# Performance work log

Hardware: AMD Instinct MI355X
Metric: run time of the kernel (lower is better)

## Reference

```python
import jax, jax.numpy as jnp
import numpy as np

DIMS = [1024, 2048, 1024, 1024]


def setup_inputs() -> dict:
    key = jax.random.key(0)
    ks = jax.random.split(key, 13)
    d_in, h1, h2, d_out = DIMS
    s = lambda k, shape, fan_in: jax.random.normal(k, shape, dtype=jnp.float32) / np.sqrt(fan_in)
    return {
        "x": jax.random.normal(ks[0], (4, 2048, d_in), dtype=jnp.float32),
        "w1": s(ks[1], (h1, d_in), d_in), "b1": jnp.zeros((h1,), jnp.float32),
        "w2": s(ks[2], (h2, h1), h1), "b2": jnp.zeros((h2,), jnp.float32),
        "wq": s(ks[3], (h2, h2), h2), "bq": jnp.zeros((h2,), jnp.float32),
        "wk": s(ks[4], (h2, h2), h2), "bk": jnp.zeros((h2,), jnp.float32),
        "wv": s(ks[5], (h2, h2), h2), "bv": jnp.zeros((h2,), jnp.float32),
        "wo": s(ks[6], (d_out, h2), h2), "bo": jnp.zeros((d_out,), jnp.float32),
    }


def reference(x, w1, b1, w2, b2, wq, bq, wk, bk, wv, bv, wo, bo):
    # MLP: Linear + ReLU twice (torch Linear: x @ W^T + b)
    h = jax.nn.relu(jnp.einsum('bsd,hd->bsh', x, w1) + b1)
    h = jax.nn.relu(jnp.einsum('bsh,eh->bse', h, w2) + b2)
    # Self-attention (single head over full hidden_dim)
    q = jnp.einsum('bse,fe->bsf', h, wq) + bq
    k = jnp.einsum('bse,fe->bsf', h, wk) + bk
    v = jnp.einsum('bse,fe->bsf', h, wv) + bv
    hidden_dim = wq.shape[0]
    scores = jnp.einsum('bsf,btf->bst', q, k) / jnp.sqrt(jnp.float32(hidden_dim))
    attn = jax.nn.softmax(scores, axis=-1)
    ctx = jnp.einsum('bst,btf->bsf', attn, v) + v  # residual with V
    return jnp.einsum('bsf,of->bso', ctx, wo) + bo
```

## Files before the change

### kernel.cpp

```cpp
#include <hip/hip_runtime.h>
#include <hip/hip_bf16.h>

typedef __bf16 bf16;
typedef bf16 bf16x8 __attribute__((ext_vector_type(8)));
typedef float f32x4 __attribute__((ext_vector_type(4)));

#define EPI_BIAS_RELU  0
#define EPI_BIAS_BF16  1
#define EPI_PLAIN_BF16 2
#define EPI_RESID      3
#define EPI_BIAS_F32   4

__device__ __forceinline__ void lds_load16(const bf16* g, bf16* l) {
  __builtin_amdgcn_global_load_lds((__attribute__((address_space(1))) void*)g,
                                   (__attribute__((address_space(3))) void*)l,
                                   16, 0, 0);
}

template<int N> __device__ __forceinline__ void vmw() {
  if constexpr (N == 0) asm volatile("s_waitcnt vmcnt(0)" ::: "memory");
  else if constexpr (N == 2) asm volatile("s_waitcnt vmcnt(2)" ::: "memory");
  else if constexpr (N == 4) asm volatile("s_waitcnt vmcnt(4)" ::: "memory");
  else if constexpr (N == 6) asm volatile("s_waitcnt vmcnt(6)" ::: "memory");
}
__device__ __forceinline__ void barrier() { asm volatile("s_barrier" ::: "memory"); }

__device__ __forceinline__ void xcd_map(int& bx, int& by, int& z) {
  const int gx = gridDim.x, gy = gridDim.y;
  const int Y8 = (gy * gridDim.z) >> 3;
  const int L = (blockIdx.z * gy + blockIdx.y) * gx + blockIdx.x;
  const int xcd = L & 7, j = L >> 3;
  bx = j % gx;
  const int yy = xcd * Y8 + j / gx;
  by = yy % gy;
  z  = yy / gy;
}

template<int EPI>
__global__ __launch_bounds__(512, 2)
void gemm4p(const bf16* __restrict__ A, const bf16* __restrict__ B,
            void* __restrict__ Cv, const float* __restrict__ bias,
            int K, int lda, int ldb, int ldc,
            long long sAz, long long sBz, long long sCz)
{
  constexpr int BM = 256, BK = 64;
  constexpr int M_REP = 8, N_REP = 4, MH = 4, NH = 2;
  constexpr int LA = 2, LB = 2, N3 = LA + LB + LA;

  __shared__ __align__(16) bf16 lA[2][BM * BK];
  __shared__ __align__(16) bf16 lB[2][256 * BK];

  int bx, by, z;
  xcd_map(bx, by, z);

  const bf16* Ab = A + (size_t)z * sAz;
  const bf16* Bb = B + (size_t)z * sBz;
  const int row0 = by * BM, col0 = bx * 256;
  const int tid = threadIdx.x, w = tid >> 6, l = tid & 63;
  const int wr = w >> 2, wc = w & 3;

  const int srow = l >> 3, scb = (l & 7) ^ srow;
  const bf16* gA = Ab + (size_t)(row0 + w * 8 + srow) * lda + scb * 8;
  const bf16* gB = Bb + (size_t)(col0 + w * 8 + srow) * ldb + scb * 8;

  auto issueA = [&](int buf, int k0, int h) {
#pragma unroll
    for (int i = 0; i < LA; i++)
      lds_load16(gA + (size_t)(h * 128 + i * 64) * lda + k0,
                 &lA[buf][(h * 128 + i * 64 + w * 8) * BK]);
  };
  auto issueB = [&](int buf, int k0, int h) {
#pragma unroll
    for (int i = 0; i < LB; i++)
      lds_load16(gB + (size_t)(h * 128 + i * 64) * ldb + k0,
                 &lB[buf][(h * 128 + i * 64 + w * 8) * BK]);
  };

  const int fr = l & 15, fq = l >> 4, sw = fr & 7;
  bf16x8 aA0[MH][2], aA1[MH][2], bB0[NH][2], bB1[NH][2];
  f32x4 acc[M_REP][N_REP] = {};

  auto readA = [&](bf16x8 (&dst)[MH][2], int buf, int h) {
#pragma unroll
    for (int mm = 0; mm < MH; mm++) {
      const bf16* base = &lA[buf][(h * 128 + wr * 64 + mm * 16 + fr) * BK];
#pragma unroll
      for (int kk = 0; kk < 2; kk++)
        dst[mm][kk] = *(const bf16x8*)(base + ((kk * 4 + fq) ^ sw) * 8);
    }
  };
  auto readB = [&](bf16x8 (&dst)[NH][2], int buf, int h) {
#pragma unroll
    for (int nn = 0; nn < NH; nn++) {
      const bf16* base = &lB[buf][(h * 128 + wc * 32 + nn * 16 + fr) * BK];
#pragma unroll
      for (int kk = 0; kk < 2; kk++)
        dst[nn][kk] = *(const bf16x8*)(base + ((kk * 4 + fq) ^ sw) * 8);
    }
  };
  auto quad = [&](const bf16x8 (&a)[MH][2], const bf16x8 (&b)[NH][2],
                  int mBase, int nBase) {
    __builtin_amdgcn_s_setprio(1);
#pragma unroll
    for (int mh = 0; mh < MH; mh++)
#pragma unroll
      for (int nh = 0; nh < NH; nh++)
#pragma unroll
        for (int kk = 0; kk < 2; kk++)
          acc[mBase + mh][nBase + nh] = __builtin_amdgcn_mfma_f32_16x16x32_bf16(
              a[mh][kk], b[nh][kk], acc[mBase + mh][nBase + nh], 0, 0, 0);
    __builtin_amdgcn_s_setprio(0);
  };

  const int NT = K / BK;
  issueA(0, 0, 0); issueB(0, 0, 0); issueA(0, 0, 1); issueB(0, 0, 1);
  issueA(1, BK, 0); issueB(1, BK, 0); issueA(1, BK, 1);
  vmw<N3>();
  barrier();

  for (int t = 0; t < NT; t++) {
    const int cur = t & 1, nxt = cur ^ 1;
    const bool s1 = (t + 1 < NT), s2 = (t + 2 < NT);
    const int k1 = (t + 1) * BK, k2 = (t + 2) * BK;
    readA(aA0, cur, 0);
    readB(bB0, cur, 0);
    if (s1) issueB(nxt, k1, 1);
    barrier();
    quad(aA0, bB0, 0, 0);
    barrier();
    readA(aA1, cur, 1);
    if (s2) issueA(cur, k2, 0);
    barrier();
    quad(aA1, bB0, MH, 0);
    barrier();
    readB(bB1, cur, 1);
    if (s2) issueB(cur, k2, 0);
    barrier();
    quad(aA1, bB1, MH, NH);
    barrier();
    if (s2) { issueA(cur, k2, 1); vmw<N3>(); }
    else vmw<0>();
    barrier();
    quad(aA0, bB1, 0, NH);
    barrier();
  }

#pragma unroll
  for (int m = 0; m < M_REP; m++) {
#pragma unroll
    for (int n = 0; n < N_REP; n++) {
      const int col = col0 + (n / NH) * 128 + wc * 32 + (n % NH) * 16 + fr;
#pragma unroll
      for (int j = 0; j < 4; j++) {
        const int rrow = row0 + (m / MH) * 128 + wr * 64 + (m % MH) * 16 + fq * 4 + j;
        const float val = acc[m][n][j];
        if constexpr (EPI == EPI_PLAIN_BF16) {
          bf16* Cp = (bf16*)Cv + (size_t)z * sCz;
          Cp[(size_t)rrow * ldc + col] = (bf16)val;
        } else if constexpr (EPI == EPI_BIAS_BF16) {
          bf16* Cp = (bf16*)Cv;
          Cp[(size_t)rrow * ldc + col] = (bf16)(val + bias[col]);
        } else if constexpr (EPI == EPI_BIAS_RELU) {
          bf16* Cp = (bf16*)Cv;
          Cp[(size_t)rrow * ldc + col] = (bf16)fmaxf(val + bias[col], 0.f);
        }
      }
    }
  }
}

template<int EPI>
__global__ __launch_bounds__(512, 2)
void gemm2p(const bf16* __restrict__ A, const bf16* __restrict__ B,
            void* __restrict__ Cv, const float* __restrict__ bias,
            const bf16* __restrict__ resid,
            int K, int lda, int ldb, int ldc, int ldr,
            long long sAz, long long sBz, long long sCz, long long sRz)
{
  constexpr int BM = 128, BK = 64;
  constexpr int M_REP = 4, NH = 2;

  __shared__ __align__(16) bf16 lA[2][BM * BK];
  __shared__ __align__(16) bf16 lB[2][256 * BK];

  int bx, by, z;
  xcd_map(bx, by, z);

  const bf16* Ab = A + (size_t)z * sAz;
  const bf16* Bb = B + (size_t)z * sBz;
  const int row0 = by * BM, col0 = bx * 256;
  const int tid = threadIdx.x, w = tid >> 6, l = tid & 63;
  const int wr = w >> 2, wc = w & 3;

  const int srow = l >> 3, scb = (l & 7) ^ srow;
  const bf16* gA = Ab + (size_t)(row0 + w * 8 + srow) * lda + scb * 8;
  const bf16* gB = Bb + (size_t)(col0 + w * 8 + srow) * ldb + scb * 8;

  auto issueAfull = [&](int buf, int k0) {
#pragma unroll
    for (int i = 0; i < 2; i++)
      lds_load16(gA + (size_t)(i * 64) * lda + k0,
                 &lA[buf][(i * 64 + w * 8) * BK]);
  };
  auto issueBfull = [&](int buf, int k0) {
#pragma unroll
    for (int i = 0; i < 4; i++)
      lds_load16(gB + (size_t)(i * 64) * ldb + k0,
                 &lB[buf][(i * 64 + w * 8) * BK]);
  };

  const int fr = l & 15, fq = l >> 4, sw = fr & 7;
  bf16x8 aA[M_REP][2], bB0[NH][2], bB1[NH][2];
  f32x4 acc[M_REP][4] = {};

  auto readAfull = [&](int buf) {
#pragma unroll
    for (int m = 0; m < M_REP; m++) {
      const bf16* base = &lA[buf][(wr * 64 + m * 16 + fr) * BK];
#pragma unroll
      for (int kk = 0; kk < 2; kk++)
        aA[m][kk] = *(const bf16x8*)(base + ((kk * 4 + fq) ^ sw) * 8);
    }
  };
  auto readB = [&](bf16x8 (&dst)[NH][2], int buf, int h) {
#pragma unroll
    for (int nn = 0; nn < NH; nn++) {
      const bf16* base = &lB[buf][(h * 128 + wc * 32 + nn * 16 + fr) * BK];
#pragma unroll
      for (int kk = 0; kk < 2; kk++)
        dst[nn][kk] = *(const bf16x8*)(base + ((kk * 4 + fq) ^ sw) * 8);
    }
  };
  auto quad2 = [&](const bf16x8 (&b)[NH][2], int nBase) {
    __builtin_amdgcn_s_setprio(1);
#pragma unroll
    for (int m = 0; m < M_REP; m++)
#pragma unroll
      for (int nh = 0; nh < NH; nh++)
#pragma unroll
        for (int kk = 0; kk < 2; kk++)
          acc[m][nBase + nh] = __builtin_amdgcn_mfma_f32_16x16x32_bf16(
              aA[m][kk], b[nh][kk], acc[m][nBase + nh], 0, 0, 0);
    __builtin_amdgcn_s_setprio(0);
  };

  const int NT = K / BK;
  issueAfull(0, 0); issueBfull(0, 0); issueAfull(1, BK);
  vmw<2>();
  barrier();

  for (int t = 0; t < NT; t++) {
    const int cur = t & 1, nxt = cur ^ 1;
    const bool s1 = (t + 1 < NT), s2 = (t + 2 < NT);
    readAfull(cur);
    readB(bB0, cur, 0);
    if (s1) issueBfull(nxt, (t + 1) * BK);
    barrier();
    quad2(bB0, 0);
    barrier();
    readB(bB1, cur, 1);
    if (s2) { issueAfull(cur, (t + 2) * BK); vmw<2>(); }
    else vmw<0>();
    barrier();
    quad2(bB1, NH);
    barrier();
  }

#pragma unroll
  for (int m = 0; m < M_REP; m++) {
#pragma unroll
    for (int n = 0; n < 4; n++) {
      const int col = col0 + (n / NH) * 128 + wc * 32 + (n % NH) * 16 + fr;
#pragma unroll
      for (int j = 0; j < 4; j++) {
        const int rrow = row0 + wr * 64 + m * 16 + fq * 4 + j;
        const float val = acc[m][n][j];
        if constexpr (EPI == EPI_PLAIN_BF16) {
          bf16* Cp = (bf16*)Cv + (size_t)z * sCz;
          Cp[(size_t)rrow * ldc + col] = (bf16)val;
        } else if constexpr (EPI == EPI_BIAS_F32) {
          float* Cp = (float*)Cv;
          Cp[(size_t)rrow * ldc + col] = val + bias[col];
        } else if constexpr (EPI == EPI_BIAS_BF16) {
          bf16* Cp = (bf16*)Cv;
          Cp[(size_t)rrow * ldc + col] = (bf16)(val + bias[col]);
        } else if constexpr (EPI == EPI_BIAS_RELU) {
          bf16* Cp = (bf16*)Cv;
          Cp[(size_t)rrow * ldc + col] = (bf16)fmaxf(val + bias[col], 0.f);
        } else {
          bf16* Cp = (bf16*)Cv + (size_t)z * sCz;
          const bf16* Rp = resid + (size_t)z * sRz;
          Cp[(size_t)rrow * ldc + col] = (bf16)(val + (float)Rp[(size_t)rrow * ldr + col]);
        }
      }
    }
  }
}

__global__ __launch_bounds__(256)
void cast_all(const float* __restrict__ x,  const float* __restrict__ w1,
              const float* __restrict__ w2, const float* __restrict__ wq,
              const float* __restrict__ wk, const float* __restrict__ wv,
              const float* __restrict__ wo,
              bf16* __restrict__ xb, bf16* __restrict__ w1b,
              bf16* __restrict__ w2b, bf16* __restrict__ wqkb,
              bf16* __restrict__ wvb, bf16* __restrict__ wob) {
  const int b = blockIdx.x;
  const float* src; bf16* dst; int base; float scale = 1.f;
  if (b < 4096)      { src = x;  dst = xb;   base = b; }
  else if (b < 5120) { src = w1; dst = w1b;  base = b - 4096; }
  else if (b < 6144) { src = w2; dst = w2b;  base = b - 5120; }
  else if (b < 6656) { src = wq; dst = wqkb;              base = b - 6144; scale = 0.03125f; }
  else if (b < 7168) { src = wk; dst = wqkb + (1 << 20);  base = b - 6656; }
  else if (b < 7680) { src = wv; dst = wvb;  base = b - 7168; }
  else               { src = wo; dst = wob;  base = b - 7680; }
  const int i = base * 256 + threadIdx.x;
  const float4* p = (const float4*)src;
  float4 a = p[2 * i], c = p[2 * i + 1];
  bf16x8 o8;
  o8[0] = (bf16)(a.x * scale); o8[1] = (bf16)(a.y * scale);
  o8[2] = (bf16)(a.z * scale); o8[3] = (bf16)(a.w * scale);
  o8[4] = (bf16)(c.x * scale); o8[5] = (bf16)(c.y * scale);
  o8[6] = (bf16)(c.z * scale); o8[7] = (bf16)(c.w * scale);
  ((bf16x8*)dst)[i] = o8;
}

__global__ __launch_bounds__(256)
void pack_bias_qk(const float* __restrict__ bq, const float* __restrict__ bk,
                  float* __restrict__ o) {
  int i = blockIdx.x * 256 + threadIdx.x;
  o[i] = (i < 1024) ? bq[i] * 0.03125f : bk[i - 1024];
}

__global__ __launch_bounds__(256)
void transpose_bf16(const bf16* __restrict__ in, bf16* __restrict__ out,
                    int R, int C, int ldi,
                    long long inZ, long long outZ) {
  __shared__ bf16 t[64][72];
  const bf16* ib = in + (size_t)blockIdx.z * inZ;
  bf16* ob = out + (size_t)blockIdx.z * outZ;
  const int r0 = blockIdx.y * 64, c0 = blockIdx.x * 64;
  const int tid = threadIdx.x;
#pragma unroll
  for (int p = 0; p < 2; p++) {
    int r = p * 32 + tid / 8, cc = (tid % 8) * 8;
    bf16x8 vv = *(const bf16x8*)(ib + (size_t)(r0 + r) * ldi + c0 + cc);
#pragma unroll
    for (int j = 0; j < 8; j++) t[r][cc + j] = vv[j];
  }
  __syncthreads();
#pragma unroll
  for (int p = 0; p < 2; p++) {
    int r = p * 32 + tid / 8, cc = (tid % 8) * 8;
    bf16x8 o;
#pragma unroll
    for (int j = 0; j < 8; j++) o[j] = t[cc + j][r];
    *(bf16x8*)(ob + (size_t)(c0 + r) * R + r0 + cc) = o;
  }
}

__global__ __launch_bounds__(256)
void softmax_rows(bf16* __restrict__ S) {
  const size_t row = blockIdx.x;
  const int t = threadIdx.x, wv_ = t >> 6, ln = t & 63;
  bf16x8 v8 = ((const bf16x8*)(S + row * 2048))[t];
  float v[8];
#pragma unroll
  for (int j = 0; j < 8; j++) v[j] = (float)v8[j];
  float m = v[0];
#pragma unroll
  for (int j = 1; j < 8; j++) m = fmaxf(m, v[j]);
  for (int o = 32; o; o >>= 1) m = fmaxf(m, __shfl_xor(m, o));
  __shared__ float redm[4], reds[4];
  if (ln == 0) redm[wv_] = m;
  __syncthreads();
  m = fmaxf(fmaxf(redm[0], redm[1]), fmaxf(redm[2], redm[3]));
  float e[8], s = 0.f;
#pragma unroll
  for (int j = 0; j < 8; j++) { e[j] = __expf(v[j] - m); s += e[j]; }
  for (int o = 32; o; o >>= 1) s += __shfl_xor(s, o);
  if (ln == 0) reds[wv_] = s;
  __syncthreads();
  s = reds[0] + reds[1] + reds[2] + reds[3];
  const float inv = 1.f / s;
  bf16x8 o8;
#pragma unroll
  for (int j = 0; j < 8; j++) o8[j] = (bf16)(e[j] * inv);
  ((bf16x8*)(S + row * 2048))[t] = o8;
}

extern "C" void kernel_launch(void* const* d_in, const int* in_sizes, int n_in,
                              void* d_out, int out_size, void* d_ws, size_t ws_size,
                              hipStream_t stream) {
  const float* x  = (const float*)d_in[0];
  const float* w1 = (const float*)d_in[1];
  const float* b1 = (const float*)d_in[2];
  const float* w2 = (const float*)d_in[3];
  const float* b2 = (const float*)d_in[4];
  const float* wq = (const float*)d_in[5];
  const float* bq = (const float*)d_in[6];
  const float* wk = (const float*)d_in[7];
  const float* bk = (const float*)d_in[8];
  const float* wv = (const float*)d_in[9];
  const float* bv = (const float*)d_in[10];
  const float* wo = (const float*)d_in[11];
  const float* bo = (const float*)d_in[12];
  float* out = (float*)d_out;

  char* ws = (char*)d_ws;
  const size_t MB = 1024ull * 1024ull;
  if (ws_size < 130 * MB) return;

  bf16* w1b  = (bf16*)(ws + 0 * MB);
  bf16* w2b  = (bf16*)(ws + 4 * MB);
  bf16* wqkb = (bf16*)(ws + 8 * MB);
  bf16* wvb  = (bf16*)(ws + 12 * MB);
  bf16* wob  = (bf16*)(ws + 14 * MB);
  float* bqk = (float*)(ws + 16 * MB);
  bf16* xb  = (bf16*)(ws + 17 * MB);
  bf16* h1  = (bf16*)(ws + 33 * MB);
  bf16* h   = (bf16*)(ws + 65 * MB);
  bf16* qk  = (bf16*)(ws + 81 * MB);
  bf16* vb  = (bf16*)(ws + 113 * MB);
  bf16* vT  = (bf16*)(ws + 17 * MB);
  bf16* S   = (bf16*)(ws + 33 * MB);
  bf16* ctx = (bf16*)(ws + 65 * MB);

  cast_all<<<8192, 256, 0, stream>>>(x, w1, w2, wq, wk, wv, wo,
                                     xb, w1b, w2b, wqkb, wvb, wob);
  pack_bias_qk<<<8, 256, 0, stream>>>(bq, bk, bqk);

  gemm4p<EPI_BIAS_RELU><<<dim3(8, 32, 1), 512, 0, stream>>>(
      xb, w1b, h1, b1, 1024, 1024, 1024, 2048, 0, 0, 0);
  gemm2p<EPI_BIAS_RELU><<<dim3(4, 64, 1), 512, 0, stream>>>(
      h1, w2b, h, b2, nullptr, 2048, 2048, 2048, 1024, 0, 0, 0, 0, 0);
  gemm4p<EPI_BIAS_BF16><<<dim3(8, 32, 1), 512, 0, stream>>>(
      h, wqkb, qk, bqk, 1024, 1024, 1024, 2048, 0, 0, 0);
  gemm2p<EPI_BIAS_BF16><<<dim3(4, 64, 1), 512, 0, stream>>>(
      h, wvb, vb, bv, nullptr, 1024, 1024, 1024, 1024, 0, 0, 0, 0, 0);
  transpose_bf16<<<dim3(16, 32, 4), 256, 0, stream>>>(
      vb, vT, 2048, 1024, 1024, 2048LL * 1024, 1024LL * 2048);
  gemm4p<EPI_PLAIN_BF16><<<dim3(8, 8, 4), 512, 0, stream>>>(
      qk, qk + 1024, S, nullptr, 1024, 2048, 2048, 2048,
      2048LL * 2048, 2048LL * 2048, 2048LL * 2048);
  softmax_rows<<<8192, 256, 0, stream>>>(S);
  gemm2p<EPI_RESID><<<dim3(4, 16, 4), 512, 0, stream>>>(
      S, vT, ctx, nullptr, vb, 2048, 2048, 2048, 1024, 1024,
      2048LL * 2048, 1024LL * 2048, 2048LL * 1024, 2048LL * 1024);
  gemm2p<EPI_BIAS_F32><<<dim3(4, 64, 1), 512, 0, stream>>>(
      ctx, wob, out, bo, nullptr, 1024, 1024, 1024, 1024, 0, 0, 0, 0, 0);
}
```

Before: 268.4 us.

## Replace four-phase GEMM pipeline with two-phase schedule loading full A fragments

The 256x256 GEMM kernel moves from a four-quadrant schedule (eight barriers per K-step, half-tile loads interleaved) to a two-phase schedule. Each phase reads all eight A fragments into registers once and runs 32 MFMAs against half of B. Whole A and B tiles are issued in bulk. This halves the barriers and LDS re-reads of A per K-step, at the cost of more registers for A fragments and coarser load/compute overlap.

Result: no change. 266.6 us (-0.7%).

```diff
diff --git a/kernel.cpp b/kernel.cpp
--- a/kernel.cpp
+++ b/kernel.cpp
@@ -21,7 +21,6 @@
   if constexpr (N == 0) asm volatile("s_waitcnt vmcnt(0)" ::: "memory");
   else if constexpr (N == 2) asm volatile("s_waitcnt vmcnt(2)" ::: "memory");
   else if constexpr (N == 4) asm volatile("s_waitcnt vmcnt(4)" ::: "memory");
-  else if constexpr (N == 6) asm volatile("s_waitcnt vmcnt(6)" ::: "memory");
 }
 __device__ __forceinline__ void barrier() { asm volatile("s_barrier" ::: "memory"); }
 
@@ -38,16 +37,15 @@
 
 template<int EPI>
 __global__ __launch_bounds__(512, 2)
-void gemm4p(const bf16* __restrict__ A, const bf16* __restrict__ B,
+void gemm2x(const bf16* __restrict__ A, const bf16* __restrict__ B,
             void* __restrict__ Cv, const float* __restrict__ bias,
             int K, int lda, int ldb, int ldc,
             long long sAz, long long sBz, long long sCz)
 {
-  constexpr int BM = 256, BK = 64;
-  constexpr int M_REP = 8, N_REP = 4, MH = 4, NH = 2;
-  constexpr int LA = 2, LB = 2, N3 = LA + LB + LA;
-
-  __shared__ __align__(16) bf16 lA[2][BM * BK];
+  constexpr int BK = 64;
+  constexpr int M_REP = 8, N_REP = 4, NH = 2;
+
+  __shared__ __align__(16) bf16 lA[2][256 * BK];
   __shared__ __align__(16) bf16 lB[2][256 * BK];
 
   int bx, by, z;
@@ -55,7 +53,7 @@
 
   const bf16* Ab = A + (size_t)z * sAz;
   const bf16* Bb = B + (size_t)z * sBz;
-  const int row0 = by * BM, col0 = bx * 256;
+  const int row0 = by * 256, col0 = bx * 256;
   const int tid = threadIdx.x, w = tid >> 6, l = tid & 63;
   const int wr = w >> 2, wc = w & 3;
 
@@ -63,30 +61,31 @@
   const bf16* gA = Ab + (size_t)(row0 + w * 8 + srow) * lda + scb * 8;
   const bf16* gB = Bb + (size_t)(col0 + w * 8 + srow) * ldb + scb * 8;
 
-  auto issueA = [&](int buf, int k0, int h) {
-#pragma unroll
-    for (int i = 0; i < LA; i++)
-      lds_load16(gA + (size_t)(h * 128 + i * 64) * lda + k0,
-                 &lA[buf][(h * 128 + i * 64 + w * 8) * BK]);
-  };
-  auto issueB = [&](int buf, int k0, int h) {
-#pragma unroll
-    for (int i = 0; i < LB; i++)
-      lds_load16(gB + (size_t)(h * 128 + i * 64) * ldb + k0,
-                 &lB[buf][(h * 128 + i * 64 + w * 8) * BK]);
+  auto issueA = [&](int buf, int k0) {
+#pragma unroll
+    for (int i = 0; i < 4; i++)
+      lds_load16(gA + (size_t)(i * 64) * lda + k0,
+                 &lA[buf][(i * 64 + w * 8) * BK]);
+  };
+  auto issueB = [&](int buf, int k0) {
+#pragma unroll
+    for (int i = 0; i < 4; i++)
+      lds_load16(gB + (size_t)(i * 64) * ldb + k0,
+                 &lB[buf][(i * 64 + w * 8) * BK]);
   };
 
   const int fr = l & 15, fq = l >> 4, sw = fr & 7;
-  bf16x8 aA0[MH][2], aA1[MH][2], bB0[NH][2], bB1[NH][2];
+  bf16x8 aA[M_REP][2], bB0[NH][2], bB1[NH][2];
   f32x4 acc[M_REP][N_REP] = {};
 
-  auto readA = [&](bf16x8 (&dst)[MH][2], int buf, int h) {
-#pragma unroll
-    for (int mm = 0; mm < MH; mm++) {
-      const bf16* base = &lA[buf][(h * 128 + wr * 64 + mm * 16 + fr) * BK];
+  auto readAfull = [&](int buf) {
+#pragma unroll
+    for (int m = 0; m < M_REP; m++) {
+      const int r = (m >> 2) * 128 + wr * 64 + (m & 3) * 16 + fr;
+      const bf16* base = &lA[buf][r * BK];
 #pragma unroll
       for (int kk = 0; kk < 2; kk++)
-        dst[mm][kk] = *(const bf16x8*)(base + ((kk * 4 + fq) ^ sw) * 8);
+        aA[m][kk] = *(const bf16x8*)(base + ((kk * 4 + fq) ^ sw) * 8);
     }
   };
   auto readB = [&](bf16x8 (&dst)[NH][2], int buf, int h) {
@@ -98,50 +97,38 @@
         dst[nn][kk] = *(const bf16x8*)(base + ((kk * 4 + fq) ^ sw) * 8);
     }
   };
-  auto quad = [&](const bf16x8 (&a)[MH][2], const bf16x8 (&b)[NH][2],
-                  int mBase, int nBase) {
+  auto quad32 = [&](const bf16x8 (&b)[NH][2], int nBase) {
     __builtin_amdgcn_s_setprio(1);
 #pragma unroll
-    for (int mh = 0; mh < MH; mh++)
+    for (int m = 0; m < M_REP; m++)
 #pragma unroll
       for (int nh = 0; nh < NH; nh++)
 #pragma unroll
         for (int kk = 0; kk < 2; kk++)
-          acc[mBase + mh][nBase + nh] = __builtin_amdgcn_mfma_f32_16x16x32_bf16(
-              a[mh][kk], b[nh][kk], acc[mBase + mh][nBase + nh], 0, 0, 0);
+          acc[m][nBase + nh] = __builtin_amdgcn_mfma_f32_16x16x32_bf16(
+              aA[m][kk], b[nh][kk], acc[m][nBase + nh], 0, 0, 0);
     __builtin_amdgcn_s_setprio(0);
   };
 
   const int NT = K / BK;
-  issueA(0, 0, 0); issueB(0, 0, 0); issueA(0, 0, 1); issueB(0, 0, 1);
-  issueA(1, BK, 0); issueB(1, BK, 0); issueA(1, BK, 1);
-  vmw<N3>();
+  issueA(0, 0); issueB(0, 0); issueA(1, BK);
+  vmw<4>();
   barrier();
 
   for (int t = 0; t < NT; t++) {
     const int cur = t & 1, nxt = cur ^ 1;
     const bool s1 = (t + 1 < NT), s2 = (t + 2 < NT);
-    const int k1 = (t + 1) * BK, k2 = (t + 2) * BK;
-    readA(aA0, cur, 0);
+    readAfull(cur);
     readB(bB0, cur, 0);
-    if (s1) issueB(nxt, k1, 1);
-    barrier();
-    quad(aA0, bB0, 0, 0);
-    barrier();
-    readA(aA1, cur, 1);
-    if (s2) issueA(cur, k2, 0);
-    barrier();
-    quad(aA1, bB0, MH, 0);
+    if (s1) issueB(nxt, (t + 1) * BK);
+    barrier();
+    quad32(bB0, 0);
     barrier();
     readB(bB1, cur, 1);
-    if (s2) issueB(cur, k2, 0);
-    barrier();
-    quad(aA1, bB1, MH, NH);
-    barrier();
-    if (s2) { issueA(cur, k2, 1); vmw<N3>(); }
+    if (s2) { issueA(cur, (t + 2) * BK); vmw<4>(); }
     else vmw<0>();
     barrier();
-    quad(aA0, bB1, 0, NH);
+    quad32(bB1, NH);
     barrier();
   }
 
@@ -152,7 +139,7 @@
       const int col = col0 + (n / NH) * 128 + wc * 32 + (n % NH) * 16 + fr;
 #pragma unroll
       for (int j = 0; j < 4; j++) {
-        const int rrow = row0 + (m / MH) * 128 + wr * 64 + (m % MH) * 16 + fq * 4 + j;
+        const int rrow = row0 + (m >> 2) * 128 + wr * 64 + (m & 3) * 16 + fq * 4 + j;
         const float val = acc[m][n][j];
         if constexpr (EPI == EPI_PLAIN_BF16) {
           bf16* Cp = (bf16*)Cv + (size_t)z * sCz;
@@ -430,17 +417,17 @@
                                      xb, w1b, w2b, wqkb, wvb, wob);
   pack_bias_qk<<<8, 256, 0, stream>>>(bq, bk, bqk);
 
-  gemm4p<EPI_BIAS_RELU><<<dim3(8, 32, 1), 512, 0, stream>>>(
+  gemm2x<EPI_BIAS_RELU><<<dim3(8, 32, 1), 512, 0, stream>>>(
       xb, w1b, h1, b1, 1024, 1024, 1024, 2048, 0, 0, 0);
   gemm2p<EPI_BIAS_RELU><<<dim3(4, 64, 1), 512, 0, stream>>>(
       h1, w2b, h, b2, nullptr, 2048, 2048, 2048, 1024, 0, 0, 0, 0, 0);
-  gemm4p<EPI_BIAS_BF16><<<dim3(8, 32, 1), 512, 0, stream>>>(
+  gemm2x<EPI_BIAS_BF16><<<dim3(8, 32, 1), 512, 0, stream>>>(
       h, wqkb, qk, bqk, 1024, 1024, 1024, 2048, 0, 0, 0);
   gemm2p<EPI_BIAS_BF16><<<dim3(4, 64, 1), 512, 0, stream>>>(
       h, wvb, vb, bv, nullptr, 1024, 1024, 1024, 1024, 0, 0, 0, 0, 0);
   transpose_bf16<<<dim3(16, 32, 4), 256, 0, stream>>>(
       vb, vT, 2048, 1024, 1024, 2048LL * 1024, 1024LL * 2048);
-  gemm4p<EPI_PLAIN_BF16><<<dim3(8, 8, 4), 512, 0, stream>>>(
+  gemm2x<EPI_PLAIN_BF16><<<dim3(8, 8, 4), 512, 0, stream>>>(
       qk, qk + 1024, S, nullptr, 1024, 2048, 2048, 2048,
       2048LL * 2048, 2048LL * 2048, 2048LL * 2048);
   softmax_rows<<<8192, 256, 0, stream>>>(S);
```
